# Performance work log

Hardware: AMD Instinct MI355X
Metric: run time of the kernel (lower is better)

The kernel has to match this reference:

```python
import jax, jax.numpy as jnp
import numpy as np
from jax import lax

N = 300000
PRE_NMS_TOP_K = 6000   # mode == 'test'
POST_NMS_TOP_K = 300   # mode == 'test'
IOU_THR = 0.7
MIN_SIZE = 1.0 / 1000.0


def setup_inputs() -> dict:
    key = jax.random.key(0)
    k1, k2, k3, k4 = jax.random.split(key, 4)
    cls = jax.random.normal(k1, (N, 2), dtype=jnp.float32)
    reg = jax.random.normal(k2, (N, 4), dtype=jnp.float32) * 0.2
    # anchors: random centers in [0,1], sizes in [0.01, 0.21], stored as (x1,y1,x2,y2)
    centers = jax.random.uniform(k3, (N, 2), dtype=jnp.float32)
    sizes = jax.random.uniform(k4, (N, 2), dtype=jnp.float32) * 0.2 + 0.01
    anchor = jnp.concatenate([centers - sizes / 2, centers + sizes / 2], axis=-1)
    return {"cls": cls, "reg": reg, "anchor": anchor}


def _xy_to_cxcy(xy):
    return jnp.concatenate([(xy[:, :2] + xy[:, 2:]) / 2, xy[:, 2:] - xy[:, :2]], axis=-1)


def _cxcy_to_xy(cxcy):
    return jnp.concatenate([cxcy[:, :2] - cxcy[:, 2:] / 2, cxcy[:, :2] + cxcy[:, 2:] / 2], axis=-1)


def _decode(reg, anchor_cxcy):
    cxcy = reg[:, :2] * anchor_cxcy[:, 2:] + anchor_cxcy[:, :2]
    wh = jnp.exp(reg[:, 2:]) * anchor_cxcy[:, 2:]
    return jnp.concatenate([cxcy, wh], axis=-1)


def _iou_matrix(b):
    # b: [K,4] xyxy -> [K,K] pairwise IoU
    area = (b[:, 2] - b[:, 0]) * (b[:, 3] - b[:, 1])
    lt = jnp.maximum(b[:, None, :2], b[None, :, :2])
    rb = jnp.minimum(b[:, None, 2:], b[None, :, 2:])
    wh = jnp.clip(rb - lt, 0.0)
    inter = wh[..., 0] * wh[..., 1]
    return inter / (area[:, None] + area[None, :] - inter + 1e-9)


def reference(cls, reg, anchor):
    scores = jax.nn.softmax(cls, axis=-1)[:, 1]                      # [N]
    roi = _cxcy_to_xy(_decode(reg, _xy_to_cxcy(anchor)))
    roi = jnp.clip(roi, 0.0, 1.0)                                    # [N,4]
    ws = roi[:, 2] - roi[:, 0]
    hs = roi[:, 3] - roi[:, 1]
    valid = (hs >= MIN_SIZE) & (ws >= MIN_SIZE)
    # filter-by-masking: invalid boxes get -inf score so they sort last
    masked_scores = jnp.where(valid, scores, -jnp.inf)
    top_scores, top_idx = lax.top_k(masked_scores, PRE_NMS_TOP_K)    # descending
    boxes = roi[top_idx]                                             # [K,4]
    valid_k = jnp.isfinite(top_scores)                               # [K]

    iou = _iou_matrix(boxes)                                         # [K,K]
    K = PRE_NMS_TOP_K
    col = jnp.arange(K)

    def body(keep, xs):
        i, row = xs
        suppress = (row > IOU_THR) & (col > i) & keep[i]
        return keep & (~suppress), None

    keep, _ = lax.scan(body, valid_k, (jnp.arange(K), iou))

    # first POST_NMS_TOP_K kept boxes in score order (stable sort puts kept first)
    order = jnp.argsort((~keep).astype(jnp.int32), stable=True)
    sel = order[:POST_NMS_TOP_K]
    out = boxes[sel] * keep[sel][:, None].astype(boxes.dtype)        # zero-pad unkept slots
    return out
```

## Files before the change

### kernel.cpp

```cpp
#include <hip/hip_runtime.h>
#include <stdint.h>

#pragma clang fp contract(off)

#define NN    300000
#define TOPK  6000u
#define KW    94
#define KPAD  6016
#define SORTN 8192
#define NCHUNK 16
#define CSZ   512
#define OUTK  300
#define ECAP2 2048
#define NREP  8

static constexpr size_t OFF_ROI    = 0;
static constexpr size_t OFF_KEY    = OFF_ROI + (size_t)NN * 16;
static constexpr size_t OFF_HIST16 = ((OFF_KEY + (size_t)NN * 4 + 255) & ~(size_t)255);
static constexpr size_t OFF_SCAL   = OFF_HIST16 + (size_t)NREP * 65536 * 4;
static constexpr size_t OFF_ECNT   = OFF_SCAL + 256;
static constexpr size_t ZERO_BYTES = (OFF_ECNT + 512) - OFF_HIST16;
static constexpr size_t OFF_HISTS  = OFF_ECNT + 512;
static constexpr size_t OFF_BSUM   = OFF_HISTS + 65536 * 4;
static constexpr size_t OFF_SORT   = OFF_BSUM + 1024;
static constexpr size_t OFF_SELBOX = OFF_SORT + (size_t)SORTN * 8;
static constexpr size_t OFF_DIAG   = ((OFF_SELBOX + (size_t)KPAD * 16 + 255) & ~(size_t)255);
static constexpr size_t OFF_ELIST  = OFF_DIAG + (size_t)KPAD * 8;


static constexpr uint32_t ZG = (uint32_t)(ZERO_BYTES / 16);
static constexpr uint32_t INIT_BLOCKS = (ZG + 255) / 256;

__device__ __forceinline__ uint32_t score_key(float s) {
  uint32_t u = __float_as_uint(s);
  u = (u >> 31) ? ~u : (u | 0x80000000u);
  return ~u;
}
__device__ __forceinline__ uint32_t hslot(uint32_t b) { return __brev(b) >> 16; }

__global__ void __launch_bounds__(256) k_init(char* __restrict__ ws) {
  uint32_t idx = blockIdx.x * 256 + threadIdx.x;
  if (idx < ZG)
    ((uint4*)(ws + OFF_HIST16))[idx] = make_uint4(0u, 0u, 0u, 0u);
}

__global__ void k_decode(const float* __restrict__ cls, const float* __restrict__ reg,
                         const float* __restrict__ anchor, float4* __restrict__ roi,
                         uint32_t* __restrict__ key, uint32_t* __restrict__ hist16) {
  int i = blockIdx.x * blockDim.x + threadIdx.x;
  if (i >= NN) return;
  float c0 = cls[2 * i], c1 = cls[2 * i + 1];
  float m  = fmaxf(c0, c1);
  float a0 = c0 - m, a1 = c1 - m;
  float tn = fminf(a0, a1);
  float e  = (float)exp((double)tn);
  float e0 = (a0 == 0.0f) ? 1.0f : e;
  float e1 = (a1 == 0.0f) ? 1.0f : e;
  float s  = e1 / (e0 + e1);

  float4 a = ((const float4*)anchor)[i];
  float acx = (a.x + a.z) * 0.5f;
  float acy = (a.y + a.w) * 0.5f;
  float aw  = a.z - a.x;
  float ah  = a.w - a.y;
  float4 r = ((const float4*)reg)[i];
  float cx = r.x * aw + acx;
  float cy = r.y * ah + acy;
  float w  = (float)exp((double)r.z) * aw;
  float h  = (float)exp((double)r.w) * ah;
  float x1 = cx - w * 0.5f, y1 = cy - h * 0.5f;
  float x2 = cx + w * 0.5f, y2 = cy + h * 0.5f;
  x1 = fminf(fmaxf(x1, 0.0f), 1.0f);
  y1 = fminf(fmaxf(y1, 0.0f), 1.0f);
  x2 = fminf(fmaxf(x2, 0.0f), 1.0f);
  y2 = fminf(fmaxf(y2, 0.0f), 1.0f);
  float ws_ = x2 - x1, hs_ = y2 - y1;
  bool valid = (hs_ >= 0.001f) && (ws_ >= 0.001f);
  float msc = valid ? s : -__builtin_inff();
  uint32_t kk = score_key(msc);

  roi[i] = make_float4(x1, y1, x2, y2);
  key[i] = kk;
  if (valid) atomicAdd(&hist16[((blockIdx.x & (NREP - 1)) << 16) + hslot(kk >> 16)], 1u);
}

__global__ void __launch_bounds__(256) k_hsumS(const uint32_t* __restrict__ hist16,
                                               uint32_t* __restrict__ hists,
                                               uint32_t* __restrict__ bsum,
                                               int* __restrict__ scal) {
  __shared__ uint32_t red[256];
  __shared__ uint32_t cum[256];
  __shared__ int Bs;
  __shared__ int lastblk;
  int t = threadIdx.x;
  int b = blockIdx.x * 256 + t;
  uint32_t slot = hslot((uint32_t)b);
  uint32_t s = 0;
#pragma unroll
  for (int r = 0; r < NREP; r++) s += hist16[(r << 16) + slot];
  hists[b] = s;
  red[t] = s;
  __syncthreads();
  for (int off = 128; off > 0; off >>= 1) {
    if (t < off) red[t] += red[t + off];
    __syncthreads();
  }
  if (t == 0) bsum[blockIdx.x] = red[0];

  __syncthreads();
  if (t == 0) {
    __threadfence();
    uint32_t old = atomicAdd((uint32_t*)&scal[8], 1u);
    lastblk = (old == (uint32_t)(gridDim.x - 1));
  }
  __syncthreads();
  if (!lastblk) return;
  __threadfence();

  uint32_t v = bsum[t];
  cum[t] = v;
  if (t == 0) Bs = 256;
  __syncthreads();
  for (int off = 1; off < 256; off <<= 1) {
    uint32_t x = (t >= off) ? cum[t - off] : 0;
    __syncthreads();
    cum[t] += x;
    __syncthreads();
  }
  if (t == 255) scal[4] = (int)cum[255];
  if (cum[t] >= TOPK && (t == 0 || cum[t - 1] < TOPK)) Bs = t;
  __syncthreads();
  int B = Bs;
  if (B == 256) { if (t == 0) scal[0] = 65535; return; }
  uint32_t cumbase = (B > 0) ? cum[B - 1] : 0;
  __syncthreads();
  uint32_t h2 = hists[B * 256 + t];
  cum[t] = h2;
  __syncthreads();
  for (int off = 1; off < 256; off <<= 1) {
    uint32_t x = (t >= off) ? cum[t - off] : 0;
    __syncthreads();
    cum[t] += x;
    __syncthreads();
  }
  uint32_t cc = cumbase + cum[t];
  uint32_t cp = cc - h2;
  if (cc >= TOPK && cp < TOPK) scal[0] = B * 256 + t;
}

__global__ void k_compact(const uint32_t* __restrict__ key, int* __restrict__ scal,
                          unsigned long long* __restrict__ sortbuf) {
  __shared__ int lcnt, lbase;
  int t = threadIdx.x;
  int i = blockIdx.x * blockDim.x + t;
  if (t == 0) lcnt = 0;
  __syncthreads();
  bool sel = false;
  uint32_t kk = 0;
  int my = 0;
  if (i < NN) {
    uint32_t P = (uint32_t)scal[0];
    kk = key[i];
    if ((kk >> 16) <= P) { sel = true; my = atomicAdd(&lcnt, 1); }
  }
  __syncthreads();
  if (t == 0 && lcnt > 0) lbase = atomicAdd(&scal[3], lcnt);
  __syncthreads();
  if (sel) {
    int pos = lbase + my;
    if (pos < SORTN) sortbuf[pos] = (((unsigned long long)kk) << 32) | (uint32_t)i;
  }
}

__global__ void __launch_bounds__(256) k_sortA(unsigned long long* __restrict__ sortbuf,
                                               const int* __restrict__ scal) {
  __shared__ unsigned long long sm[CSZ];
  int t = threadIdx.x;
  int total = scal[3];
  if (total > SORTN) total = SORTN;
  unsigned long long* chunk = sortbuf + (size_t)blockIdx.x * CSZ;
  int g0 = blockIdx.x * CSZ + t;
  sm[t] = (g0 < total) ? chunk[t] : ~0ull;
  sm[t + 256] = (g0 + 256 < total) ? chunk[t + 256] : ~0ull;
  __syncthreads();
  for (int k = 2; k <= CSZ; k <<= 1) {
    for (int j = k >> 1; j > 0; j >>= 1) {
      int i1 = ((t & ~(j - 1)) << 1) | (t & (j - 1));
      int i2 = i1 | j;
      bool up = ((i1 & k) == 0);
      unsigned long long a = sm[i1], b = sm[i2];
      if ((a > b) == up) { sm[i1] = b; sm[i2] = a; }
      __syncthreads();
    }
  }
  chunk[t] = sm[t];
  chunk[t + 256] = sm[t + 256];
}

__global__ void __launch_bounds__(256) k_sortB(const unsigned long long* __restrict__ sortbuf,
                                               const float4* __restrict__ roi,
                                               float4* __restrict__ selbox) {
  int gt = blockIdx.x * 256 + threadIdx.x;
  int e  = gt >> 4;
  int c2 = gt & 15;
  int c  = e >> 9;
  unsigned long long val = sortbuf[e];
  const unsigned long long* base = sortbuf + ((size_t)c2 << 9);
  bool le = (c2 < c);
  uint32_t pos = 0;
#pragma unroll
  for (int s = CSZ; s > 0; s >>= 1) {
    if (pos + s <= CSZ) {
      unsigned long long v = base[pos + s - 1];
      if (le ? (v <= val) : (v < val)) pos += s;
    }
  }
  uint32_t rank = pos;
#pragma unroll
  for (int off = 8; off > 0; off >>= 1) rank += __shfl_xor(rank, off, 16);
  if (c2 == 0) {
    if (rank < TOPK) {
      uint32_t bi = (uint32_t)val;
      selbox[rank] = (bi < NN) ? roi[bi] : make_float4(0.f, 0.f, 0.f, 0.f);
    } else if (rank < KPAD) {
      selbox[rank] = make_float4(0.f, 0.f, 0.f, 0.f);
    }
  }
}

__global__ void __launch_bounds__(64) k_mask(const float4* __restrict__ selbox,
                                             unsigned long long* __restrict__ diag,
                                             uint32_t* __restrict__ ecnt,
                                             uint32_t* __restrict__ elist) {
  int bi = blockIdx.x, bj = blockIdx.y;
  if (bj < bi) return;
  int t = threadIdx.x;
  __shared__ float4 jb[64];
  __shared__ float  ja[64];
  int j0 = bj * 64;
  float4 cb = selbox[j0 + t];
  jb[t] = cb;
  ja[t] = (cb.z - cb.x) * (cb.w - cb.y);
  __syncthreads();
  int i = bi * 64 + t;
  unsigned long long word = 0;
  if (i < (int)TOPK) {
    float4 bi4 = selbox[i];
    float ai = (bi4.z - bi4.x) * (bi4.w - bi4.y);
    for (int jj = 0; jj < 64; jj++) {
      int j = j0 + jj;
      float4 bb = jb[jj];
      float ltx = fmaxf(bi4.x, bb.x), lty = fmaxf(bi4.y, bb.y);
      float rbx = fminf(bi4.z, bb.z), rby = fminf(bi4.w, bb.w);
      float wx = fmaxf(rbx - ltx, 0.0f), wy = fmaxf(rby - lty, 0.0f);
      float inter = wx * wy;
      float iou = inter / (ai + ja[jj] - inter + 1e-9f);
      if (iou > 0.7f && j > i && j < (int)TOPK) word |= (1ull << jj);
    }
  }
  if (bi == bj) {
    diag[i] = word;
    return;
  }
  uint32_t cnt = (uint32_t)__popcll(word);
  uint32_t pre = cnt;
#pragma unroll
  for (int off = 1; off < 64; off <<= 1) {
    uint32_t v = __shfl_up(pre, off);
    if (t >= off) pre += v;
  }
  uint32_t total = __shfl(pre, 63);
  if (total == 0) return;
  uint32_t excl = pre - cnt;
  uint32_t base;
  if (t == 0) base = atomicAdd(&ecnt[bi], total);
  base = __shfl(base, 0);
  unsigned long long rem = word;
  uint32_t k = 0;
  while (rem) {
    int jj = (int)__builtin_ctzll(rem);
    rem &= rem - 1;
    uint32_t pos = base + excl + k;
    k++;
    if (pos < ECAP2) elist[(size_t)bi * ECAP2 + pos] = ((uint32_t)i << 16) | (uint32_t)(j0 + jj);
  }
}

__global__ void __launch_bounds__(256) k_seq(const unsigned long long* __restrict__ diag,
                                             const uint32_t* __restrict__ ecnt,
                                             const uint32_t* __restrict__ elist,
                                             const int* __restrict__ scal,
                                             const float4* __restrict__ selbox,
                                             float* __restrict__ out) {
  __shared__ uint32_t pend32[2 * KW];
  __shared__ uint32_t keep32[2 * KW];
  __shared__ uint32_t wcnt_s[KW], wrank[KW], carry_s;
  const int t = threadIdx.x, lane = t & 63;

  if (t < 2 * KW) pend32[t] = 0;
  __syncthreads();

  if (t < 64) {
    uint32_t ec0 = ecnt[lane];
    ec0 = (ec0 > ECAP2) ? ECAP2 : ec0;
    uint32_t ec1 = 0;
    if (64 + lane < KW) {
      ec1 = ecnt[64 + lane];
      ec1 = (ec1 > ECAP2) ? ECAP2 : ec1;
    }
    int V = scal[4];
    if (V > (int)TOPK) V = (int)TOPK;

    unsigned long long mb = diag[lane];
    uint32_t cw = __builtin_amdgcn_readlane(ec0, 0);
    uint32_t en0 = elist[lane];
    uint32_t en1 = elist[64 + lane];

    uint32_t cum = 0;
    int cut = KW - 1;
    for (int c = 0; c < KW; c++) {
      unsigned long long mbn = 0;
      uint32_t cwn = 0, en0n = 0, en1n = 0;
      if (c + 1 < KW) {
        mbn = diag[(c + 1) * 64 + lane];
        cwn = (c + 1 < 64) ? __builtin_amdgcn_readlane(ec0, c + 1)
                           : __builtin_amdgcn_readlane(ec1, c + 1 - 64);
        en0n = elist[(size_t)(c + 1) * ECAP2 + lane];
        en1n = elist[(size_t)(c + 1) * ECAP2 + 64 + lane];
      }
      uint32_t plo = pend32[2 * c], phi = pend32[2 * c + 1];
      int d = V - c * 64;
      unsigned long long vinit =
          (d <= 0) ? 0ull : ((d >= 64) ? ~0ull : ((1ull << d) - 1));
      unsigned long long w = vinit & ~(((unsigned long long)phi << 32) | plo);
      unsigned long long sup = __ballot(mb != 0);
      unsigned long long rem = w & sup;
      while (rem) {
        int b = (int)__builtin_ctzll(rem);
        uint32_t mlo = __builtin_amdgcn_readlane((uint32_t)mb, b);
        uint32_t mhi = __builtin_amdgcn_readlane((uint32_t)(mb >> 32), b);
        w &= ~(((unsigned long long)mhi << 32) | mlo);
        rem = (b >= 63) ? 0ull : (w & sup & (~0ull << (b + 1)));
      }
      if (lane == 0) {
        keep32[2 * c] = (uint32_t)w;
        keep32[2 * c + 1] = (uint32_t)(w >> 32);
      }
      cum += (uint32_t)__popcll(w);
      if (cum >= OUTK) { cut = c; break; }
      if ((uint32_t)lane < cw) {
        uint32_t i = en0 >> 16, j = en0 & 0xFFFFu;
        if ((w >> (i & 63)) & 1ull) atomicOr(&pend32[j >> 5], 1u << (j & 31));
      }
      if ((uint32_t)(64 + lane) < cw) {
        uint32_t i = en1 >> 16, j = en1 & 0xFFFFu;
        if ((w >> (i & 63)) & 1ull) atomicOr(&pend32[j >> 5], 1u << (j & 31));
      }
      for (uint32_t k = 128 + (uint32_t)lane; k < cw; k += 64) {
        uint32_t e = elist[(size_t)c * ECAP2 + k];
        uint32_t i = e >> 16, j = e & 0xFFFFu;
        if ((w >> (i & 63)) & 1ull) atomicOr(&pend32[j >> 5], 1u << (j & 31));
      }
      mb = mbn; cw = cwn; en0 = en0n; en1 = en1n;
    }
    for (int wz = cut + 1 + lane; wz < KW; wz += 64) {
      keep32[2 * wz] = 0;
      keep32[2 * wz + 1] = 0;
    }
  }
  __syncthreads();

  if (t < KW)
    wcnt_s[t] = (uint32_t)(__popc(keep32[2 * t]) + __popc(keep32[2 * t + 1]));
  __syncthreads();
  if (t < 64) {
    uint32_t v = wcnt_s[t], p2 = v;
#pragma unroll
    for (int off = 1; off < 64; off <<= 1) {
      uint32_t x = __shfl_up(p2, off);
      if (lane >= off) p2 += x;
    }
    wrank[t] = p2 - v;
    if (t == 63) carry_s = p2;
  }
  __syncthreads();
  if (t >= 64 && t < KW) {
    uint32_t v = wcnt_s[t], p2 = v;
#pragma unroll
    for (int off = 1; off < 64; off <<= 1) {
      uint32_t x = __shfl_up(p2, off);
      if (lane >= off) p2 += x;
    }
    wrank[t] = carry_s + p2 - v;
  }
  __syncthreads();
  for (int o = t; o < OUTK * 4; o += 256) out[o] = 0.0f;
  __syncthreads();
  for (int r = t; r < (int)TOPK; r += 256) {
    unsigned long long w =
        ((unsigned long long)keep32[2 * (r >> 6) + 1] << 32) | keep32[2 * (r >> 6)];
    int b = r & 63;
    if ((w >> b) & 1ull) {
      uint32_t rank = wrank[r >> 6] + (uint32_t)__popcll(w & ((1ull << b) - 1ull));
      if (rank < OUTK) {
        float4 bx = selbox[r];
        out[rank * 4 + 0] = bx.x;
        out[rank * 4 + 1] = bx.y;
        out[rank * 4 + 2] = bx.z;
        out[rank * 4 + 3] = bx.w;
      }
    }
  }
}

extern "C" void kernel_launch(void* const* d_in, const int* in_sizes, int n_in,
                              void* d_out, int out_size, void* d_ws, size_t ws_size,
                              hipStream_t stream) {
  const float* cls    = (const float*)d_in[0];
  const float* reg    = (const float*)d_in[1];
  const float* anchor = (const float*)d_in[2];
  float* out = (float*)d_out;
  char* ws = (char*)d_ws;

  float4*   roi     = (float4*)(ws + OFF_ROI);
  uint32_t* key     = (uint32_t*)(ws + OFF_KEY);
  uint32_t* hist16  = (uint32_t*)(ws + OFF_HIST16);
  uint32_t* hists   = (uint32_t*)(ws + OFF_HISTS);
  uint32_t* bsum    = (uint32_t*)(ws + OFF_BSUM);
  int*      scal    = (int*)(ws + OFF_SCAL);
  uint32_t* ecnt    = (uint32_t*)(ws + OFF_ECNT);
  unsigned long long* sortbuf = (unsigned long long*)(ws + OFF_SORT);
  float4*   selbox  = (float4*)(ws + OFF_SELBOX);
  unsigned long long* diag = (unsigned long long*)(ws + OFF_DIAG);
  uint32_t* elist   = (uint32_t*)(ws + OFF_ELIST);

  int blocks = (NN + 255) / 256;
  k_init<<<INIT_BLOCKS, 256, 0, stream>>>(ws);
  k_decode<<<blocks, 256, 0, stream>>>(cls, reg, anchor, roi, key, hist16);
  k_hsumS<<<256, 256, 0, stream>>>(hist16, hists, bsum, scal);
  k_compact<<<blocks, 256, 0, stream>>>(key, scal, sortbuf);
  k_sortA<<<NCHUNK, 256, 0, stream>>>(sortbuf, scal);
  k_sortB<<<SORTN * 16 / 256, 256, 0, stream>>>(sortbuf, roi, selbox);
  k_mask<<<dim3(KW, KW), 64, 0, stream>>>(selbox, diag, ecnt, elist);
  k_seq<<<1, 256, 0, stream>>>(diag, ecnt, elist, scal, selbox, out);
}
```

Baseline: 89.96 us.

## Replace bitonic chunk sort plus merge-rank with single brute-force counting rank kernel

Removes the two-kernel sort (per-chunk bitonic sort in LDS followed by binary-search merge ranking) and replaces it with one kernel that computes each candidate's rank by counting all smaller keys, streamed through LDS tiles. This drops a kernel launch and the serial bitonic phase that ran on only 16 blocks, trading them for O(n^2) comparisons spread across 256 blocks. Padding slots past the candidate count are now zeroed by index instead of by rank.

Result: slower. 113.2 us (+25.8%).

```diff
diff --git a/kernel.cpp b/kernel.cpp
--- a/kernel.cpp
+++ b/kernel.cpp
@@ -8,11 +8,10 @@
 #define KW    94
 #define KPAD  6016
 #define SORTN 8192
-#define NCHUNK 16
-#define CSZ   512
 #define OUTK  300
 #define ECAP2 2048
 #define NREP  8
+#define NBLK  256
 
 static constexpr size_t OFF_ROI    = 0;
 static constexpr size_t OFF_KEY    = OFF_ROI + (size_t)NN * 16;
@@ -172,58 +171,44 @@
   }
 }
 
-__global__ void __launch_bounds__(256) k_sortA(unsigned long long* __restrict__ sortbuf,
-                                               const int* __restrict__ scal) {
-  __shared__ unsigned long long sm[CSZ];
-  int t = threadIdx.x;
+__global__ void __launch_bounds__(256) k_rank(const unsigned long long* __restrict__ sortbuf,
+                                              const int* __restrict__ scal,
+                                              const float4* __restrict__ roi,
+                                              float4* __restrict__ selbox) {
+  __shared__ unsigned long long tile[2048];
+  const int t = threadIdx.x;
   int total = scal[3];
   if (total > SORTN) total = SORTN;
-  unsigned long long* chunk = sortbuf + (size_t)blockIdx.x * CSZ;
-  int g0 = blockIdx.x * CSZ + t;
-  sm[t] = (g0 < total) ? chunk[t] : ~0ull;
-  sm[t + 256] = (g0 + 256 < total) ? chunk[t + 256] : ~0ull;
-  __syncthreads();
-  for (int k = 2; k <= CSZ; k <<= 1) {
-    for (int j = k >> 1; j > 0; j >>= 1) {
-      int i1 = ((t & ~(j - 1)) << 1) | (t & (j - 1));
-      int i2 = i1 | j;
-      bool up = ((i1 & k) == 0);
-      unsigned long long a = sm[i1], b = sm[i2];
-      if ((a > b) == up) { sm[i1] = b; sm[i2] = a; }
-      __syncthreads();
-    }
-  }
-  chunk[t] = sm[t];
-  chunk[t + 256] = sm[t + 256];
-}
-
-__global__ void __launch_bounds__(256) k_sortB(const unsigned long long* __restrict__ sortbuf,
-                                               const float4* __restrict__ roi,
-                                               float4* __restrict__ selbox) {
-  int gt = blockIdx.x * 256 + threadIdx.x;
-  int e  = gt >> 4;
-  int c2 = gt & 15;
-  int c  = e >> 9;
-  unsigned long long val = sortbuf[e];
-  const unsigned long long* base = sortbuf + ((size_t)c2 << 9);
-  bool le = (c2 < c);
-  uint32_t pos = 0;
+  int e = blockIdx.x * 32 + (t >> 3);
+  int sub = t & 7;
+  bool real = (e < total);
+  unsigned long long val = real ? sortbuf[e] : 0ull;
+  uint32_t cnt = 0;
+  for (int base = 0; base < SORTN; base += 2048) {
+    for (int k = t; k < 2048; k += 256) {
+      int j = base + k;
+      tile[k] = (j < total) ? sortbuf[j] : ~0ull;
+    }
+    __syncthreads();
+    if (real) {
+      int j0 = sub * 256;
+#pragma unroll 8
+      for (int k = 0; k < 256; k++)
+        cnt += (tile[j0 + k] < val) ? 1u : 0u;
+    }
+    __syncthreads();
+  }
 #pragma unroll
-  for (int s = CSZ; s > 0; s >>= 1) {
-    if (pos + s <= CSZ) {
-      unsigned long long v = base[pos + s - 1];
-      if (le ? (v <= val) : (v < val)) pos += s;
-    }
-  }
-  uint32_t rank = pos;
-#pragma unroll
-  for (int off = 8; off > 0; off >>= 1) rank += __shfl_xor(rank, off, 16);
-  if (c2 == 0) {
-    if (rank < TOPK) {
-      uint32_t bi = (uint32_t)val;
-      selbox[rank] = (bi < NN) ? roi[bi] : make_float4(0.f, 0.f, 0.f, 0.f);
-    } else if (rank < KPAD) {
-      selbox[rank] = make_float4(0.f, 0.f, 0.f, 0.f);
+  for (int off = 4; off > 0; off >>= 1) cnt += __shfl_xor(cnt, off, 8);
+  if (sub == 0) {
+    if (real) {
+      if (cnt < TOPK) {
+        selbox[cnt] = roi[(uint32_t)val];
+      } else if (cnt < KPAD) {
+        selbox[cnt] = make_float4(0.f, 0.f, 0.f, 0.f);
+      }
+    } else if (e < KPAD) {
+      selbox[e] = make_float4(0.f, 0.f, 0.f, 0.f);
     }
   }
 }
@@ -437,10 +422,9 @@
   int blocks = (NN + 255) / 256;
   k_init<<<INIT_BLOCKS, 256, 0, stream>>>(ws);
   k_decode<<<blocks, 256, 0, stream>>>(cls, reg, anchor, roi, key, hist16);
-  k_hsumS<<<256, 256, 0, stream>>>(hist16, hists, bsum, scal);
+  k_hsumS<<<NBLK, 256, 0, stream>>>(hist16, hists, bsum, scal);
   k_compact<<<blocks, 256, 0, stream>>>(key, scal, sortbuf);
-  k_sortA<<<NCHUNK, 256, 0, stream>>>(sortbuf, scal);
-  k_sortB<<<SORTN * 16 / 256, 256, 0, stream>>>(sortbuf, roi, selbox);
+  k_rank<<<SORTN / 32, 256, 0, stream>>>(sortbuf, scal, roi, selbox);
   k_mask<<<dim3(KW, KW), 64, 0, stream>>>(selbox, diag, ecnt, elist);
   k_seq<<<1, 256, 0, stream>>>(diag, ecnt, elist, scal, selbox, out);
 }
```

## Limit precomputed IoU mask to first 16 word-rows, compute later rows on demand

Applied to the files above, without the earlier changes.

The pairwise IoU mask kernel now only processes the first 16 row-blocks (1024 boxes) instead of all 94, since the top 300 kept boxes usually come from early candidates. If the sequential NMS has not reached 300 kept boxes after those rows, a fallback path in the single-block kernel computes IoUs directly against the already-kept boxes and within each 64-box word. This removes most of the quadratic mask work. The cost is a slow serial fallback when many boxes are suppressed or invalid.

New measurement: 82.85 us. -7.9%, faster.

```diff
diff --git a/kernel.cpp b/kernel.cpp
--- a/kernel.cpp
+++ b/kernel.cpp
@@ -13,6 +13,8 @@
 #define OUTK  300
 #define ECAP2 2048
 #define NREP  8
+#define NBLK  256
+#define CUTW  16
 
 static constexpr size_t OFF_ROI    = 0;
 static constexpr size_t OFF_KEY    = OFF_ROI + (size_t)NN * 16;
@@ -37,6 +39,9 @@
   return ~u;
 }
 __device__ __forceinline__ uint32_t hslot(uint32_t b) { return __brev(b) >> 16; }
+__device__ __forceinline__ float rlf(float v, int l) {
+  return __uint_as_float(__builtin_amdgcn_readlane(__float_as_uint(v), l));
+}
 
 __global__ void __launch_bounds__(256) k_init(char* __restrict__ ws) {
   uint32_t idx = blockIdx.x * 256 + threadIdx.x;
@@ -296,18 +301,14 @@
   __shared__ uint32_t keep32[2 * KW];
   __shared__ uint32_t wcnt_s[KW], wrank[KW], carry_s;
   const int t = threadIdx.x, lane = t & 63;
+  const int NW = (KW < CUTW) ? KW : CUTW;
 
   if (t < 2 * KW) pend32[t] = 0;
   __syncthreads();
 
   if (t < 64) {
-    uint32_t ec0 = ecnt[lane];
+    uint32_t ec0 = (lane < NW) ? ecnt[lane] : 0;
     ec0 = (ec0 > ECAP2) ? ECAP2 : ec0;
-    uint32_t ec1 = 0;
-    if (64 + lane < KW) {
-      ec1 = ecnt[64 + lane];
-      ec1 = (ec1 > ECAP2) ? ECAP2 : ec1;
-    }
     int V = scal[4];
     if (V > (int)TOPK) V = (int)TOPK;
 
@@ -318,13 +319,14 @@
 
     uint32_t cum = 0;
     int cut = KW - 1;
-    for (int c = 0; c < KW; c++) {
+    bool done = false;
+
+    for (int c = 0; c < NW; c++) {
       unsigned long long mbn = 0;
       uint32_t cwn = 0, en0n = 0, en1n = 0;
-      if (c + 1 < KW) {
+      if (c + 1 < NW) {
         mbn = diag[(c + 1) * 64 + lane];
-        cwn = (c + 1 < 64) ? __builtin_amdgcn_readlane(ec0, c + 1)
-                           : __builtin_amdgcn_readlane(ec1, c + 1 - 64);
+        cwn = __builtin_amdgcn_readlane(ec0, c + 1);
         en0n = elist[(size_t)(c + 1) * ECAP2 + lane];
         en1n = elist[(size_t)(c + 1) * ECAP2 + 64 + lane];
       }
@@ -347,7 +349,7 @@
         keep32[2 * c + 1] = (uint32_t)(w >> 32);
       }
       cum += (uint32_t)__popcll(w);
-      if (cum >= OUTK) { cut = c; break; }
+      if (cum >= OUTK) { cut = c; done = true; break; }
       if ((uint32_t)lane < cw) {
         uint32_t i = en0 >> 16, j = en0 & 0xFFFFu;
         if ((w >> (i & 63)) & 1ull) atomicOr(&pend32[j >> 5], 1u << (j & 31));
@@ -362,6 +364,62 @@
         if ((w >> (i & 63)) & 1ull) atomicOr(&pend32[j >> 5], 1u << (j & 31));
       }
       mb = mbn; cw = cwn; en0 = en0n; en1 = en1n;
+    }
+
+    if (!done) {
+      for (int c = NW; c < KW; c++) {
+        int d = V - c * 64;
+        if (d <= 0) {
+          if (lane == 0) { keep32[2 * c] = 0; keep32[2 * c + 1] = 0; }
+          continue;
+        }
+        unsigned long long vinit = (d >= 64) ? ~0ull : ((1ull << d) - 1);
+        uint32_t plo = pend32[2 * c], phi = pend32[2 * c + 1];
+        unsigned long long pend = vinit & ~(((unsigned long long)phi << 32) | plo);
+        int j = c * 64 + lane;
+        float4 bx = selbox[j];
+        float aj = (bx.z - bx.x) * (bx.w - bx.y);
+        bool sup = false;
+        for (int wz = NW; wz < c; wz++) {
+          unsigned long long kw =
+              ((unsigned long long)keep32[2 * wz + 1] << 32) | keep32[2 * wz];
+          while (kw) {
+            int b = (int)__builtin_ctzll(kw);
+            kw &= kw - 1;
+            float4 kb = selbox[wz * 64 + b];
+            float ak = (kb.z - kb.x) * (kb.w - kb.y);
+            float ltx = fmaxf(kb.x, bx.x), lty = fmaxf(kb.y, bx.y);
+            float rbx = fminf(kb.z, bx.z), rby = fminf(kb.w, bx.w);
+            float wx = fmaxf(rbx - ltx, 0.0f), wy = fmaxf(rby - lty, 0.0f);
+            float inter = wx * wy;
+            float iou = inter / (ak + aj - inter + 1e-9f);
+            sup |= (iou > 0.7f);
+          }
+        }
+        pend &= ~__ballot(sup);
+        unsigned long long kmask = 0;
+        while (pend) {
+          int b = (int)__builtin_ctzll(pend);
+          kmask |= 1ull << b;
+          float bxx = rlf(bx.x, b), byy = rlf(bx.y, b);
+          float bzz = rlf(bx.z, b), bww = rlf(bx.w, b);
+          float ab  = rlf(aj, b);
+          float ltx = fmaxf(bxx, bx.x), lty = fmaxf(byy, bx.y);
+          float rbx = fminf(bzz, bx.z), rby = fminf(bww, bx.w);
+          float wx = fmaxf(rbx - ltx, 0.0f), wy = fmaxf(rby - lty, 0.0f);
+          float inter = wx * wy;
+          float iou = inter / (ab + aj - inter + 1e-9f);
+          unsigned long long suppress = __ballot(iou > 0.7f);
+          pend &= ~(1ull << b);
+          pend &= ~(suppress & (~0ull << (b + 1)));
+        }
+        if (lane == 0) {
+          keep32[2 * c] = (uint32_t)kmask;
+          keep32[2 * c + 1] = (uint32_t)(kmask >> 32);
+        }
+        cum += (uint32_t)__popcll(kmask);
+        if (cum >= OUTK) { cut = c; break; }
+      }
     }
     for (int wz = cut + 1 + lane; wz < KW; wz += 64) {
       keep32[2 * wz] = 0;
@@ -437,10 +495,10 @@
   int blocks = (NN + 255) / 256;
   k_init<<<INIT_BLOCKS, 256, 0, stream>>>(ws);
   k_decode<<<blocks, 256, 0, stream>>>(cls, reg, anchor, roi, key, hist16);
-  k_hsumS<<<256, 256, 0, stream>>>(hist16, hists, bsum, scal);
+  k_hsumS<<<NBLK, 256, 0, stream>>>(hist16, hists, bsum, scal);
   k_compact<<<blocks, 256, 0, stream>>>(key, scal, sortbuf);
   k_sortA<<<NCHUNK, 256, 0, stream>>>(sortbuf, scal);
   k_sortB<<<SORTN * 16 / 256, 256, 0, stream>>>(sortbuf, roi, selbox);
-  k_mask<<<dim3(KW, KW), 64, 0, stream>>>(selbox, diag, ecnt, elist);
+  k_mask<<<dim3(CUTW, KW), 64, 0, stream>>>(selbox, diag, ecnt, elist);
   k_seq<<<1, 256, 0, stream>>>(diag, ecnt, elist, scal, selbox, out);
 }
```
